# Optimization experiments

Measured on AMD Instinct MI355X. Metric: run time of the kernel, lower is better.

The kernel has to match this reference:

```python
import jax, jax.numpy as jnp
import numpy as np

B, T, F, H = 128, 256, 64, 512

def glorot(key, shape):
    fan_in, fan_out = shape[0], shape[1]
    lim = jnp.sqrt(6.0 / (fan_in + fan_out))
    return jax.random.uniform(key, shape, jnp.float32, -lim, lim)

def setup_inputs() -> dict:
    key = jax.random.key(0)
    ks = jax.random.split(key, 8)
    x = jax.random.normal(ks[0], (B, T, F), jnp.float32)
    W1 = glorot(ks[1], (F, H)); b1 = jnp.zeros((H,), jnp.float32)
    Wx1 = glorot(ks[2], (H, 4 * H)); Wh1 = glorot(ks[3], (H, 4 * H))
    blstm1 = jnp.concatenate([jnp.zeros((H,)), jnp.ones((H,)), jnp.zeros((2 * H,))]).astype(jnp.float32)  # keras unit_forget_bias
    Wx2 = glorot(ks[4], (H, 4 * H)); Wh2 = glorot(ks[5], (H, 4 * H))
    blstm2 = jnp.concatenate([jnp.zeros((H,)), jnp.ones((H,)), jnp.zeros((2 * H,))]).astype(jnp.float32)
    gamma = jnp.ones((H,), jnp.float32); beta = jnp.zeros((H,), jnp.float32)
    W2 = glorot(ks[6], (H, H // 2)); b2 = jnp.zeros((H // 2,), jnp.float32)
    W3 = glorot(ks[7], (H // 2, 1)); b3 = jnp.zeros((1,), jnp.float32)
    return dict(x=x, W1=W1, b1=b1, Wx1=Wx1, Wh1=Wh1, blstm1=blstm1,
                Wx2=Wx2, Wh2=Wh2, blstm2=blstm2, gamma=gamma, beta=beta,
                W2=W2, b2=b2, W3=W3, b3=b3)

def lstm(x, Wx, Wh, b):
    # x: [B, T, Din] -> sequence of hidden states [B, T, H] and last h [B, H]
    h_dim = Wh.shape[0]
    xg = jnp.einsum('btd,dg->btg', x, Wx) + b  # precompute input contributions [B,T,4H]
    def step(carry, xt):
        h, c = carry
        g = xt + h @ Wh
        i, f, cb, o = jnp.split(g, 4, axis=-1)
        i = jax.nn.sigmoid(i); f = jax.nn.sigmoid(f); o = jax.nn.sigmoid(o)
        c = f * c + i * jnp.tanh(cb)
        h = o * jnp.tanh(c)
        return (h, c), h
    init = (jnp.zeros((x.shape[0], h_dim), x.dtype), jnp.zeros((x.shape[0], h_dim), x.dtype))
    (h_last, _), hs = jax.lax.scan(step, init, jnp.swapaxes(xg, 0, 1))
    return jnp.swapaxes(hs, 0, 1), h_last

def reference(x, W1, b1, Wx1, Wh1, blstm1, Wx2, Wh2, blstm2, gamma, beta, W2, b2, W3, b3):
    h = x @ W1 + b1                                  # dense1 [B,T,H]
    # spectral_norm lambda: L2-normalize last axis, scale by sqrt(H)
    norm = jnp.linalg.norm(h, axis=-1, keepdims=True)
    h = h / jnp.maximum(norm, 1e-12) * jnp.sqrt(jnp.float32(h.shape[-1]))
    seq, _ = lstm(h, Wx1, Wh1, blstm1)               # lstm1 return_sequences
    _, h2 = lstm(seq, Wx2, Wh2, blstm2)              # lstm2 last output [B,H]
    mu = jnp.mean(h2, axis=-1, keepdims=True)
    var = jnp.mean((h2 - mu) ** 2, axis=-1, keepdims=True)
    h2 = (h2 - mu) * jax.lax.rsqrt(var + 1e-3) * gamma + beta  # keras LayerNorm eps=1e-3
    h3 = jax.nn.relu(h2 @ W2 + b2)
    return h3 @ W3 + b3                               # [B,1]
```

## Files before the change

kernel.cpp:

```cpp
#include <hip/hip_runtime.h>
#include <hip/hip_bf16.h>
#include <math.h>

#define B_ 128
#define T_ 256
#define F_ 64
#define H_ 512
#define G4_ 2048

#define XB0_OFF 0
#define XB1_OFF 32768
#define HB_OFF  65536
#define GLD_OFF 98304
#define SMEM_TOTAL 115712

typedef __attribute__((ext_vector_type(8))) short bf16x8;
typedef __attribute__((ext_vector_type(4))) float f32x4;

__device__ __forceinline__ void coh_store_u32(unsigned* p, unsigned v) {
  __hip_atomic_store(p, v, __ATOMIC_RELAXED, __HIP_MEMORY_SCOPE_AGENT);
}
__device__ __forceinline__ unsigned coh_load_u32(const unsigned* p) {
  return __hip_atomic_load(p, __ATOMIC_RELAXED, __HIP_MEMORY_SCOPE_AGENT);
}
__device__ __forceinline__ void rawbar() { __builtin_amdgcn_s_barrier(); }

__device__ __forceinline__ void async_ld16(const void* g, void* l) {
  __builtin_amdgcn_global_load_lds(
      (const __attribute__((address_space(1))) void*)g,
      (__attribute__((address_space(3))) void*)l, 16, 0, 0);
}
__device__ __forceinline__ void async_ld16c(const void* g, void* l) {
  __builtin_amdgcn_global_load_lds(
      (const __attribute__((address_space(1))) void*)g,
      (__attribute__((address_space(3))) void*)l, 16, 0, 17);
}

__device__ __forceinline__ float fsig(float x) {
  float e = __builtin_amdgcn_exp2f(-1.44269504089f * x);
  return __builtin_amdgcn_rcpf(1.f + e);
}
__device__ __forceinline__ float ftanh(float x) {
  float ax = __builtin_fabsf(x);
  float e = __builtin_amdgcn_exp2f(-2.88539008177f * ax);
  float r = (1.f - e) * __builtin_amdgcn_rcpf(1.f + e);
  return __builtin_copysignf(r, x);
}

__global__ __launch_bounds__(256) void transpose_cast_k(
    const float* __restrict__ s0, const float* __restrict__ s1,
    const float* __restrict__ s2, const float* __restrict__ s3,
    __hip_bfloat16* __restrict__ dst)
{
  __shared__ float lds[64][65];
  const float* src = (blockIdx.z == 0) ? s0 : (blockIdx.z == 1) ? s1 : (blockIdx.z == 2) ? s2 : s3;
  __hip_bfloat16* d = dst + (size_t)blockIdx.z * (G4_ * H_);
  int n0 = blockIdx.x * 64, k0 = blockIdx.y * 64;
  int tx = threadIdx.x & 63, ty = threadIdx.x >> 6;
#pragma unroll
  for (int r = 0; r < 16; r++) { int k = r * 4 + ty; lds[k][tx] = src[(size_t)(k0 + k) * G4_ + n0 + tx]; }
  __syncthreads();
#pragma unroll
  for (int r = 0; r < 16; r++) { int n = r * 4 + ty; d[(size_t)(n0 + n) * H_ + k0 + tx] = __float2bfloat16(lds[tx][n]); }
}

__global__ void prep_misc_k(const float* __restrict__ w1, __hip_bfloat16* __restrict__ w1b,
                            float* __restrict__ zbase, int nzero)
{
  int i = blockIdx.x * blockDim.x + threadIdx.x;
  int stride = gridDim.x * blockDim.x;
  for (int k = i; k < F_ * H_; k += stride) w1b[k] = __float2bfloat16(w1[k]);
  for (int k = i; k < nzero; k += stride) zbase[k] = 0.f;
}

__global__ __launch_bounds__(512) void dense1_k(
    const float* __restrict__ x, const __hip_bfloat16* __restrict__ w1b,
    const float* __restrict__ b1, __hip_bfloat16* __restrict__ h0)
{
  __shared__ float red[8];
  int j = threadIdx.x;
  int wave = j >> 6, lane = j & 63;
  float wcol[64];
#pragma unroll
  for (int k = 0; k < 64; k++) wcol[k] = __bfloat162float(w1b[k * H_ + j]);
  float bj = b1[j];
  for (int r = 0; r < 32; r++) {
    int row = blockIdx.x * 32 + r;
    const float* xr = x + (size_t)row * F_;
    float acc = bj;
#pragma unroll
    for (int k = 0; k < 64; k++) acc += xr[k] * wcol[k];
    float ss = acc * acc;
#pragma unroll
    for (int o = 32; o; o >>= 1) ss += __shfl_down(ss, o);
    if (lane == 0) red[wave] = ss;
    __syncthreads();
    float tot = red[0] + red[1] + red[2] + red[3] + red[4] + red[5] + red[6] + red[7];
    float sc = sqrtf(512.f) / fmaxf(sqrtf(tot), 1e-12f);
    h0[(size_t)row * H_ + j] = __float2bfloat16(acc * sc);
    __syncthreads();
  }
}

#define RUN_CHAIN(BASEPTR, W0, W1, A0, A1)                                    \
  {                                                                           \
    const char* _cb = (const char*)(BASEPTR);                                 \
    _Pragma("unroll")                                                         \
    for (int kc = 0; kc < 8; kc++) {                                          \
      bf16x8 _av = *(const bf16x8*)(_cb + ((mh * 16 + kh * 8 + kc) << 10) + (lane << 4)); \
      A0 = __builtin_amdgcn_mfma_f32_16x16x32_bf16(_av, W0[kc], A0, 0, 0, 0); \
      A1 = __builtin_amdgcn_mfma_f32_16x16x32_bf16(_av, W1[kc], A1, 0, 0, 0); \
    }                                                                         \
  }

__global__ __launch_bounds__(512, 2) void lstm_fused_k(
    const __hip_bfloat16* __restrict__ h0,
    __hip_bfloat16* __restrict__ seq,
    const __hip_bfloat16* __restrict__ wh1, const __hip_bfloat16* __restrict__ wx1,
    const float* __restrict__ bl1,
    const __hip_bfloat16* __restrict__ wh2, const __hip_bfloat16* __restrict__ wx2,
    const float* __restrict__ bl2,
    __hip_bfloat16* __restrict__ h1A, __hip_bfloat16* __restrict__ h1B,
    __hip_bfloat16* __restrict__ h2A, __hip_bfloat16* __restrict__ h2B,
    float* __restrict__ h2f,
    unsigned* flags)
{
  extern __shared__ char smem[];
  float* gld = (float*)(smem + GLD_OFF);
  const int tid = threadIdx.x;
  const int wave = tid >> 6;
  const int lane = tid & 63;
  const int lr = lane & 15;
  const int lk = lane >> 4;
  const int bid = blockIdx.x;
  const int grp = bid >> 7;
  const int lid = bid & 127;
  const int bb = lid & 3;
  const int bu = lid >> 2;
  const int m0 = bb * 32;
  const int u0 = bu * 16;

  const int kh = wave >> 2;
  const int mh = (wave >> 1) & 1;
  const int gp = wave & 1;

  const __hip_bfloat16* Wht = grp ? wh2 : wh1;
  const __hip_bfloat16* Wxt = grp ? wx2 : wx1;
  const __hip_bfloat16* xsrc = grp ? (const __hip_bfloat16*)seq : h0;
  const float* bias = grp ? bl2 : bl1;
  __hip_bfloat16* hgA = grp ? h2A : h1A;
  __hip_bfloat16* hgB = grp ? h2B : h1B;
  unsigned* dflags = flags + bb * 64;
  unsigned* ownf = dflags + (grp << 5);
  const int myflag = (grp << 5) | bu;

  bf16x8 wh_0[8], wh_1[8], wx_0[8], wx_1[8];
  {
    const size_t c0 = (size_t)((gp * 2 + 0) * 512 + u0 + lr) * H_ + kh * 256 + lk * 8;
    const size_t c1 = (size_t)((gp * 2 + 1) * 512 + u0 + lr) * H_ + kh * 256 + lk * 8;
#pragma unroll
    for (int kc = 0; kc < 8; kc++) {
      wh_0[kc] = *(const bf16x8*)(Wht + c0 + kc * 32);
      wh_1[kc] = *(const bf16x8*)(Wht + c1 + kc * 32);
      wx_0[kc] = *(const bf16x8*)(Wxt + c0 + kc * 32);
      wx_1[kc] = *(const bf16x8*)(Wxt + c1 + kc * 32);
    }
#pragma unroll
    for (int kc = 0; kc < 8; kc++) {
      asm volatile("" : "+v"(wh_0[kc]), "+v"(wh_1[kc]), "+v"(wx_0[kc]), "+v"(wx_1[kc]));
    }
  }

  const int m_e = tid >> 3, up_e = tid & 7;
  float br0[2], br1[2], br2[2], br3[2];
  float2 creg = {0.f, 0.f};
  if (tid < 256) {
#pragma unroll
    for (int c = 0; c < 2; c++) {
      br0[c] = bias[0 * 512 + u0 + 2 * up_e + c];
      br1[c] = bias[1 * 512 + u0 + 2 * up_e + c];
      br2[c] = bias[2 * 512 + u0 + 2 * up_e + c];
      br3[c] = bias[3 * 512 + u0 + 2 * up_e + c];
    }
  }

  char* xb0 = smem + XB0_OFF;
  char* xb1 = smem + XB1_OFF;

  auto issue_x = [&](int t, char* xb) {
#pragma unroll
    for (int j = 0; j < 4; j++) {
      const int c = wave * 4 + j;
      const __hip_bfloat16* g = xsrc +
          ((size_t)(m0 + (c >> 4) * 16 + lr) * T_ + t) * H_ + (c & 15) * 32 + lk * 8;
      if (grp) async_ld16c(g, xb + c * 1024);
      else     async_ld16(g, xb + c * 1024);
    }
  };
  auto issue_h = [&](int u) {
#pragma unroll
    for (int j = 0; j < 4; j++) {
      const int c = wave * 4 + j;
      const int row = m0 + (c >> 4) * 16 + lr;
      const __hip_bfloat16* g;
      if (grp) {
        const __hip_bfloat16* hsrc = ((u - 1) & 1) ? hgB : hgA;
        g = hsrc + (size_t)row * H_ + (c & 15) * 32 + lk * 8;
      } else {
        g = seq + ((size_t)row * T_ + (u - 1)) * H_ + (c & 15) * 32 + lk * 8;
      }
      async_ld16c(g, smem + HB_OFF + c * 1024);
    }
  };
  auto spin32 = [&](const unsigned* base, unsigned tgt) {
    if (lane < 32) {
      const unsigned* p = base + lane;
      while (coh_load_u32(p) < tgt) __builtin_amdgcn_s_sleep(1);
    }
  };
  auto spinA = [&](int u) {
    if (lane < 32) {
      const unsigned* p = ownf + lane;
      const unsigned tgt = (unsigned)u;
      while (coh_load_u32(p) < tgt) __builtin_amdgcn_s_sleep(1);
    } else if (grp == 1 && u <= T_ - 3) {
      const unsigned* p = dflags + (lane - 32);
      const unsigned tgt = (unsigned)(u + 3);
      while (coh_load_u32(p) < tgt) __builtin_amdgcn_s_sleep(1);
    }
  };
  auto publish = [&](unsigned v) {
    if (tid == 0) coh_store_u32(&dflags[myflag], v);
  };
  auto write_gld = [&](f32x4 s0, f32x4 s1) {
    float* d0 = gld + ((kh * 4 + gp * 2 + 0) * 32 + mh * 16 + lk * 4) * 17 + lr;
    float* d1 = gld + ((kh * 4 + gp * 2 + 1) * 32 + mh * 16 + lk * 4) * 17 + lr;
#pragma unroll
    for (int r = 0; r < 4; r++) { d0[r * 17] = s0[r]; d1[r * 17] = s1[r]; }
  };
  auto elem = [&](int u, __hip_bfloat16* hout) {
    if (tid < 256) {
      float gv0[2], gv1[2], gv2[2], gv3[2];
#pragma unroll
      for (int c = 0; c < 2; c++) {
        const int o = m_e * 17 + 2 * up_e + c;
        gv0[c] = gld[(0 * 32) * 17 + o] + gld[(4 * 32) * 17 + o] + br0[c];
        gv1[c] = gld[(1 * 32) * 17 + o] + gld[(5 * 32) * 17 + o] + br1[c];
        gv2[c] = gld[(2 * 32) * 17 + o] + gld[(6 * 32) * 17 + o] + br2[c];
        gv3[c] = gld[(3 * 32) * 17 + o] + gld[(7 * 32) * 17 + o] + br3[c];
      }
      float i0 = fsig(gv0[0]), i1 = fsig(gv0[1]);
      float f0 = fsig(gv1[0]), f1 = fsig(gv1[1]);
      float cb0 = ftanh(gv2[0]), cb1 = ftanh(gv2[1]);
      float o0 = fsig(gv3[0]), o1 = fsig(gv3[1]);
      float cn0 = f0 * creg.x + i0 * cb0;
      float cn1 = f1 * creg.y + i1 * cb1;
      creg.x = cn0; creg.y = cn1;
      float hv0 = o0 * ftanh(cn0), hv1 = o1 * ftanh(cn1);
      union { __hip_bfloat16 h[2]; unsigned u32; } pk;
      pk.h[0] = __float2bfloat16(hv0);
      pk.h[1] = __float2bfloat16(hv1);
      const int row = m0 + m_e, col = u0 + 2 * up_e;
      if (grp == 0) {
        coh_store_u32((unsigned*)seq + (((size_t)row * T_ + u) * H_ + col) / 2, pk.u32);
      } else {
        coh_store_u32((unsigned*)hout + ((size_t)row * H_ + col) / 2, pk.u32);
        if (u == T_ - 1) {
          float2 hv = {hv0, hv1};
          *(float2*)(h2f + (size_t)row * H_ + col) = hv;
        }
      }
    }
  };

  f32x4 axc0 = {0.f,0.f,0.f,0.f}, axc1 = {0.f,0.f,0.f,0.f};
  f32x4 axn0, axn1, ah0, ah1;

  if (grp) spin32(dflags, 3u);
  issue_x(0, xb0);
  issue_x(1, xb1);
  asm volatile("s_waitcnt vmcnt(0)" ::: "memory");
  rawbar();
  __builtin_amdgcn_sched_barrier(0);
  RUN_CHAIN(xb0, wx_0, wx_1, axc0, axc1);
  write_gld(axc0, axc1);
  asm volatile("s_waitcnt lgkmcnt(0)" ::: "memory");
  rawbar();
  __builtin_amdgcn_sched_barrier(0);
  elem(0, hgA);
  issue_x(2, xb0);
  asm volatile("s_waitcnt vmcnt(4)" ::: "memory");
  publish(1u);
  asm volatile("s_waitcnt vmcnt(0)" ::: "memory");
  rawbar();
  __builtin_amdgcn_sched_barrier(0);
  axc0 = (f32x4){0.f,0.f,0.f,0.f}; axc1 = (f32x4){0.f,0.f,0.f,0.f};
  RUN_CHAIN(xb1, wx_0, wx_1, axc0, axc1);

  for (int u = 1; u < T_; u++) {
    __hip_bfloat16* hout = (u & 1) ? hgB : hgA;
    const bool pf = (u <= T_ - 3);

    spinA(u);
    issue_h(u);
    if (u < T_ - 1) {
      axn0 = (f32x4){0.f,0.f,0.f,0.f}; axn1 = (f32x4){0.f,0.f,0.f,0.f};
      char* xb = ((u + 1) & 1) ? xb1 : xb0;
      RUN_CHAIN(xb, wx_0, wx_1, axn0, axn1);
    }
    asm volatile("s_waitcnt vmcnt(0)" ::: "memory");
    rawbar();
    __builtin_amdgcn_sched_barrier(0);
    ah0 = (f32x4){0.f,0.f,0.f,0.f}; ah1 = (f32x4){0.f,0.f,0.f,0.f};
    RUN_CHAIN(smem + HB_OFF, wh_0, wh_1, ah0, ah1);
    write_gld(axc0 + ah0, axc1 + ah1);
    asm volatile("s_waitcnt lgkmcnt(0)" ::: "memory");
    rawbar();
    __builtin_amdgcn_sched_barrier(0);
    elem(u, hout);
    if (pf) {
      issue_x(u + 2, (u & 1) ? xb1 : xb0);
      asm volatile("s_waitcnt vmcnt(4)" ::: "memory");
      publish((unsigned)(u + 1));
      asm volatile("s_waitcnt vmcnt(0)" ::: "memory");
    } else {
      asm volatile("s_waitcnt vmcnt(0)" ::: "memory");
      publish((unsigned)(u + 1));
    }
    rawbar();
    axc0 = axn0; axc1 = axn1;
  }
}

__global__ __launch_bounds__(256) void final_k(
    const float* __restrict__ h2, const float* __restrict__ gamma, const float* __restrict__ beta,
    const float* __restrict__ W2, const float* __restrict__ b2,
    const float* __restrict__ W3, const float* __restrict__ b3, float* __restrict__ out)
{
  __shared__ float y[512];
  __shared__ float redS[4], redQ[4], redP[4];
  int b = blockIdx.x, tid = threadIdx.x;
  int wave = tid >> 6, lane = tid & 63;
  float v0 = h2[b * H_ + tid], v1 = h2[b * H_ + 256 + tid];
  float s = v0 + v1, q = v0 * v0 + v1 * v1;
#pragma unroll
  for (int o = 32; o; o >>= 1) { s += __shfl_down(s, o); q += __shfl_down(q, o); }
  if (lane == 0) { redS[wave] = s; redQ[wave] = q; }
  __syncthreads();
  float tot = redS[0] + redS[1] + redS[2] + redS[3];
  float totq = redQ[0] + redQ[1] + redQ[2] + redQ[3];
  float mu = tot * (1.f / 512.f);
  float var = totq * (1.f / 512.f) - mu * mu;
  float rs = rsqrtf(var + 1e-3f);
  y[tid]       = (v0 - mu) * rs * gamma[tid] + beta[tid];
  y[tid + 256] = (v1 - mu) * rs * gamma[tid + 256] + beta[tid + 256];
  __syncthreads();
  float acc = b2[tid];
  for (int k = 0; k < 512; k++) acc += y[k] * W2[k * 256 + tid];
  float pv = fmaxf(acc, 0.f) * W3[tid];
#pragma unroll
  for (int o = 32; o; o >>= 1) pv += __shfl_down(pv, o);
  if (lane == 0) redP[wave] = pv;
  __syncthreads();
  if (tid == 0) out[b] = redP[0] + redP[1] + redP[2] + redP[3] + b3[0];
}

extern "C" void kernel_launch(void* const* d_in, const int* in_sizes, int n_in,
                              void* d_out, int out_size, void* d_ws, size_t ws_size,
                              hipStream_t stream)
{
  (void)in_sizes; (void)n_in; (void)out_size; (void)ws_size;
  const float* x    = (const float*)d_in[0];
  const float* W1   = (const float*)d_in[1];
  const float* b1   = (const float*)d_in[2];
  const float* Wx1  = (const float*)d_in[3];
  const float* Wh1  = (const float*)d_in[4];
  const float* bl1  = (const float*)d_in[5];
  const float* Wx2  = (const float*)d_in[6];
  const float* Wh2  = (const float*)d_in[7];
  const float* bl2  = (const float*)d_in[8];
  const float* gam  = (const float*)d_in[9];
  const float* bet  = (const float*)d_in[10];
  const float* W2   = (const float*)d_in[11];
  const float* b2   = (const float*)d_in[12];
  const float* W3   = (const float*)d_in[13];
  const float* b3   = (const float*)d_in[14];

  char* p = (char*)d_ws;
  const size_t MB = 1024 * 1024;
  __hip_bfloat16* wx1t = (__hip_bfloat16*)(p + 0 * MB);
  __hip_bfloat16* wh1t = (__hip_bfloat16*)(p + 2 * MB);
  __hip_bfloat16* wx2t = (__hip_bfloat16*)(p + 4 * MB);
  __hip_bfloat16* wh2t = (__hip_bfloat16*)(p + 6 * MB);
  __hip_bfloat16* w1b  = (__hip_bfloat16*)(p + 8 * MB);
  __hip_bfloat16* h0   = (__hip_bfloat16*)(p + 9 * MB);
  __hip_bfloat16* seq  = (__hip_bfloat16*)(p + 41 * MB);
  char* st = p + 73 * MB;
  __hip_bfloat16* h1A = (__hip_bfloat16*)st;
  __hip_bfloat16* h1B = h1A + B_ * H_;
  __hip_bfloat16* h2A = h1B + B_ * H_;
  __hip_bfloat16* h2B = h2A + B_ * H_;
  float* h2f = (float*)(st + 512 * 1024);
  unsigned* flags = (unsigned*)(st + 512 * 1024 + 256 * 1024);
  int nzero = (int)((512 * 1024 + 256 * 1024 + 4096) / 4);

  transpose_cast_k<<<dim3(32, 8, 4), 256, 0, stream>>>(Wx1, Wh1, Wx2, Wh2, wx1t);
  prep_misc_k<<<256, 256, 0, stream>>>(W1, w1b, (float*)st, nzero);
  dense1_k<<<1024, 512, 0, stream>>>(x, w1b, b1, h0);

  void* args[] = { (void*)&h0, (void*)&seq,
                   (void*)&wh1t, (void*)&wx1t, (void*)&bl1,
                   (void*)&wh2t, (void*)&wx2t, (void*)&bl2,
                   (void*)&h1A, (void*)&h1B, (void*)&h2A, (void*)&h2B,
                   (void*)&h2f, (void*)&flags };
  hipLaunchCooperativeKernel((void*)lstm_fused_k, dim3(256), dim3(512), args,
                             SMEM_TOTAL, stream);

  final_k<<<128, 256, 0, stream>>>(h2f, gam, bet, W2, b2, W3, b3, (float*)d_out);
}
```

Baseline: 1.181 ms.

## Interleave gate columns per wave to do LSTM cell math in registers via swizzle

Reassigns each wave's output columns so that the four gates of a hidden unit sit in adjacent lanes. Each wave now covers the full K=512 reduction, which removes the split-K LDS staging buffer and the extra barrier before the element-wise cell update. Gate values are exchanged with ds_swizzle and each lane stores one bf16 h value. The next-step x prefetch is also issued earlier so it overlaps the h matmul. The cost is a longer serial MFMA chain per wave, narrower 16-bit stores, and redundant activation work across lanes.

```diff
diff --git a/kernel.cpp b/kernel.cpp
--- a/kernel.cpp
+++ b/kernel.cpp
@@ -11,13 +11,15 @@
 #define XB0_OFF 0
 #define XB1_OFF 32768
 #define HB_OFF  65536
-#define GLD_OFF 98304
-#define SMEM_TOTAL 115712
+#define SMEM_TOTAL 98304
 
 typedef __attribute__((ext_vector_type(8))) short bf16x8;
 typedef __attribute__((ext_vector_type(4))) float f32x4;
 
 __device__ __forceinline__ void coh_store_u32(unsigned* p, unsigned v) {
+  __hip_atomic_store(p, v, __ATOMIC_RELAXED, __HIP_MEMORY_SCOPE_AGENT);
+}
+__device__ __forceinline__ void coh_store_u16(unsigned short* p, unsigned short v) {
   __hip_atomic_store(p, v, __ATOMIC_RELAXED, __HIP_MEMORY_SCOPE_AGENT);
 }
 __device__ __forceinline__ unsigned coh_load_u32(const unsigned* p) {
@@ -45,6 +47,10 @@
   float e = __builtin_amdgcn_exp2f(-2.88539008177f * ax);
   float r = (1.f - e) * __builtin_amdgcn_rcpf(1.f + e);
   return __builtin_copysignf(r, x);
+}
+template<int PAT>
+__device__ __forceinline__ float swz(float v) {
+  return __uint_as_float(__builtin_amdgcn_ds_swizzle(__float_as_uint(v), PAT));
 }
 
 __global__ __launch_bounds__(256) void transpose_cast_k(
@@ -102,14 +108,14 @@
   }
 }
 
-#define RUN_CHAIN(BASEPTR, W0, W1, A0, A1)                                    \
+#define RUN_CHAINF(BASEPTR, W, A0, A1)                                        \
   {                                                                           \
     const char* _cb = (const char*)(BASEPTR);                                 \
     _Pragma("unroll")                                                         \
-    for (int kc = 0; kc < 8; kc++) {                                          \
-      bf16x8 _av = *(const bf16x8*)(_cb + ((mh * 16 + kh * 8 + kc) << 10) + (lane << 4)); \
-      A0 = __builtin_amdgcn_mfma_f32_16x16x32_bf16(_av, W0[kc], A0, 0, 0, 0); \
-      A1 = __builtin_amdgcn_mfma_f32_16x16x32_bf16(_av, W1[kc], A1, 0, 0, 0); \
+    for (int kc = 0; kc < 16; kc++) {                                         \
+      bf16x8 _av = *(const bf16x8*)(_cb + ((mh * 16 + kc) << 10) + (lane << 4)); \
+      if (kc & 1) A1 = __builtin_amdgcn_mfma_f32_16x16x32_bf16(_av, W[kc], A1, 0, 0, 0); \
+      else        A0 = __builtin_amdgcn_mfma_f32_16x16x32_bf16(_av, W[kc], A0, 0, 0, 0); \
     }                                                                         \
   }
 
@@ -126,7 +132,6 @@
     unsigned* flags)
 {
   extern __shared__ char smem[];
-  float* gld = (float*)(smem + GLD_OFF);
   const int tid = threadIdx.x;
   const int wave = tid >> 6;
   const int lane = tid & 63;
@@ -140,9 +145,11 @@
   const int m0 = bb * 32;
   const int u0 = bu * 16;
 
-  const int kh = wave >> 2;
-  const int mh = (wave >> 1) & 1;
-  const int gp = wave & 1;
+  const int mh = wave >> 2;
+  const int q  = wave & 3;
+  const int p  = lr & 3;
+  const int ucol = u0 + q * 4 + (lr >> 2);
+  const int pcol = p * 512 + ucol;
 
   const __hip_bfloat16* Wht = grp ? wh2 : wh1;
   const __hip_bfloat16* Wxt = grp ? wx2 : wx1;
@@ -154,35 +161,22 @@
   unsigned* ownf = dflags + (grp << 5);
   const int myflag = (grp << 5) | bu;
 
-  bf16x8 wh_0[8], wh_1[8], wx_0[8], wx_1[8];
+  bf16x8 wh_[16], wx_[16];
   {
-    const size_t c0 = (size_t)((gp * 2 + 0) * 512 + u0 + lr) * H_ + kh * 256 + lk * 8;
-    const size_t c1 = (size_t)((gp * 2 + 1) * 512 + u0 + lr) * H_ + kh * 256 + lk * 8;
-#pragma unroll
-    for (int kc = 0; kc < 8; kc++) {
-      wh_0[kc] = *(const bf16x8*)(Wht + c0 + kc * 32);
-      wh_1[kc] = *(const bf16x8*)(Wht + c1 + kc * 32);
-      wx_0[kc] = *(const bf16x8*)(Wxt + c0 + kc * 32);
-      wx_1[kc] = *(const bf16x8*)(Wxt + c1 + kc * 32);
-    }
-#pragma unroll
-    for (int kc = 0; kc < 8; kc++) {
-      asm volatile("" : "+v"(wh_0[kc]), "+v"(wh_1[kc]), "+v"(wx_0[kc]), "+v"(wx_1[kc]));
+    const __hip_bfloat16* hw = Wht + (size_t)pcol * H_ + lk * 8;
+    const __hip_bfloat16* xw = Wxt + (size_t)pcol * H_ + lk * 8;
+#pragma unroll
+    for (int kc = 0; kc < 16; kc++) {
+      wh_[kc] = *(const bf16x8*)(hw + kc * 32);
+      wx_[kc] = *(const bf16x8*)(xw + kc * 32);
+    }
+#pragma unroll
+    for (int kc = 0; kc < 16; kc++) {
+      asm volatile("" : "+v"(wh_[kc]), "+v"(wx_[kc]));
     }
   }
-
-  const int m_e = tid >> 3, up_e = tid & 7;
-  float br0[2], br1[2], br2[2], br3[2];
-  float2 creg = {0.f, 0.f};
-  if (tid < 256) {
-#pragma unroll
-    for (int c = 0; c < 2; c++) {
-      br0[c] = bias[0 * 512 + u0 + 2 * up_e + c];
-      br1[c] = bias[1 * 512 + u0 + 2 * up_e + c];
-      br2[c] = bias[2 * 512 + u0 + 2 * up_e + c];
-      br3[c] = bias[3 * 512 + u0 + 2 * up_e + c];
-    }
-  }
+  const float bias0 = bias[pcol];
+  f32x4 cst = {0.f, 0.f, 0.f, 0.f};
 
   char* xb0 = smem + XB0_OFF;
   char* xb1 = smem + XB1_OFF;
@@ -214,67 +208,58 @@
   };
   auto spin32 = [&](const unsigned* base, unsigned tgt) {
     if (lane < 32) {
-      const unsigned* p = base + lane;
-      while (coh_load_u32(p) < tgt) __builtin_amdgcn_s_sleep(1);
+      const unsigned* pp = base + lane;
+      while (coh_load_u32(pp) < tgt) __builtin_amdgcn_s_sleep(1);
     }
   };
   auto spinA = [&](int u) {
     if (lane < 32) {
-      const unsigned* p = ownf + lane;
+      const unsigned* pp = ownf + lane;
       const unsigned tgt = (unsigned)u;
-      while (coh_load_u32(p) < tgt) __builtin_amdgcn_s_sleep(1);
+      while (coh_load_u32(pp) < tgt) __builtin_amdgcn_s_sleep(1);
     } else if (grp == 1 && u <= T_ - 3) {
-      const unsigned* p = dflags + (lane - 32);
+      const unsigned* pp = dflags + (lane - 32);
       const unsigned tgt = (unsigned)(u + 3);
-      while (coh_load_u32(p) < tgt) __builtin_amdgcn_s_sleep(1);
+      while (coh_load_u32(pp) < tgt) __builtin_amdgcn_s_sleep(1);
     }
   };
   auto publish = [&](unsigned v) {
     if (tid == 0) coh_store_u32(&dflags[myflag], v);
   };
-  auto write_gld = [&](f32x4 s0, f32x4 s1) {
-    float* d0 = gld + ((kh * 4 + gp * 2 + 0) * 32 + mh * 16 + lk * 4) * 17 + lr;
-    float* d1 = gld + ((kh * 4 + gp * 2 + 1) * 32 + mh * 16 + lk * 4) * 17 + lr;
-#pragma unroll
-    for (int r = 0; r < 4; r++) { d0[r * 17] = s0[r]; d1[r * 17] = s1[r]; }
-  };
-  auto elem = [&](int u, __hip_bfloat16* hout) {
-    if (tid < 256) {
-      float gv0[2], gv1[2], gv2[2], gv3[2];
-#pragma unroll
-      for (int c = 0; c < 2; c++) {
-        const int o = m_e * 17 + 2 * up_e + c;
-        gv0[c] = gld[(0 * 32) * 17 + o] + gld[(4 * 32) * 17 + o] + br0[c];
-        gv1[c] = gld[(1 * 32) * 17 + o] + gld[(5 * 32) * 17 + o] + br1[c];
-        gv2[c] = gld[(2 * 32) * 17 + o] + gld[(6 * 32) * 17 + o] + br2[c];
-        gv3[c] = gld[(3 * 32) * 17 + o] + gld[(7 * 32) * 17 + o] + br3[c];
-      }
-      float i0 = fsig(gv0[0]), i1 = fsig(gv0[1]);
-      float f0 = fsig(gv1[0]), f1 = fsig(gv1[1]);
-      float cb0 = ftanh(gv2[0]), cb1 = ftanh(gv2[1]);
-      float o0 = fsig(gv3[0]), o1 = fsig(gv3[1]);
-      float cn0 = f0 * creg.x + i0 * cb0;
-      float cn1 = f1 * creg.y + i1 * cb1;
-      creg.x = cn0; creg.y = cn1;
-      float hv0 = o0 * ftanh(cn0), hv1 = o1 * ftanh(cn1);
-      union { __hip_bfloat16 h[2]; unsigned u32; } pk;
-      pk.h[0] = __float2bfloat16(hv0);
-      pk.h[1] = __float2bfloat16(hv1);
-      const int row = m0 + m_e, col = u0 + 2 * up_e;
-      if (grp == 0) {
-        coh_store_u32((unsigned*)seq + (((size_t)row * T_ + u) * H_ + col) / 2, pk.u32);
-      } else {
-        coh_store_u32((unsigned*)hout + ((size_t)row * H_ + col) / 2, pk.u32);
-        if (u == T_ - 1) {
-          float2 hv = {hv0, hv1};
-          *(float2*)(h2f + (size_t)row * H_ + col) = hv;
-        }
-      }
-    }
-  };
 
   f32x4 axc0 = {0.f,0.f,0.f,0.f}, axc1 = {0.f,0.f,0.f,0.f};
   f32x4 axn0, axn1, ah0, ah1;
+
+  auto elem = [&](int u, __hip_bfloat16* hout, bool with_h) {
+    float hv0 = 0.f, hv1 = 0.f, hv2 = 0.f, hv3 = 0.f;
+#pragma unroll
+    for (int r = 0; r < 4; r++) {
+      float gv = axc0[r] + axc1[r] + bias0;
+      if (with_h) gv += ah0[r] + ah1[r];
+      float act = (p == 2) ? ftanh(gv) : fsig(gv);
+      float v1 = swz<0x041F>(act);
+      float v2 = swz<0x081F>(act);
+      float v3 = swz<0x0C1F>(act);
+      float iv  = (p == 0) ? act : (p == 1) ? v1  : (p == 2) ? v2  : v3;
+      float fv  = (p == 0) ? v1  : (p == 1) ? act : (p == 2) ? v3  : v2;
+      float cbv = (p == 0) ? v2  : (p == 1) ? v3  : (p == 2) ? act : v1;
+      float ov  = (p == 0) ? v3  : (p == 1) ? v2  : (p == 2) ? v1  : act;
+      float cn = fv * cst[r] + iv * cbv;
+      cst[r] = cn;
+      float hv = ov * ftanh(cn);
+      if (r == 0) hv0 = hv; else if (r == 1) hv1 = hv;
+      else if (r == 2) hv2 = hv; else hv3 = hv;
+    }
+    float hsel = (p == 0) ? hv0 : (p == 1) ? hv1 : (p == 2) ? hv2 : hv3;
+    const int row = m0 + mh * 16 + lk * 4 + p;
+    unsigned short hb = __bfloat16_as_ushort(__float2bfloat16(hsel));
+    if (grp == 0) {
+      coh_store_u16((unsigned short*)seq + ((size_t)row * T_ + u) * H_ + ucol, hb);
+    } else {
+      coh_store_u16((unsigned short*)hout + (size_t)row * H_ + ucol, hb);
+      if (u == T_ - 1) h2f[(size_t)row * H_ + ucol] = hsel;
+    }
+  };
 
   if (grp) spin32(dflags, 3u);
   issue_x(0, xb0);
@@ -282,20 +267,15 @@
   asm volatile("s_waitcnt vmcnt(0)" ::: "memory");
   rawbar();
   __builtin_amdgcn_sched_barrier(0);
-  RUN_CHAIN(xb0, wx_0, wx_1, axc0, axc1);
-  write_gld(axc0, axc1);
-  asm volatile("s_waitcnt lgkmcnt(0)" ::: "memory");
-  rawbar();
-  __builtin_amdgcn_sched_barrier(0);
-  elem(0, hgA);
+  RUN_CHAINF(xb0, wx_, axc0, axc1);
   issue_x(2, xb0);
-  asm volatile("s_waitcnt vmcnt(4)" ::: "memory");
+  elem(0, hgA, false);
+  asm volatile("s_waitcnt vmcnt(0)" ::: "memory");
   publish(1u);
-  asm volatile("s_waitcnt vmcnt(0)" ::: "memory");
   rawbar();
   __builtin_amdgcn_sched_barrier(0);
   axc0 = (f32x4){0.f,0.f,0.f,0.f}; axc1 = (f32x4){0.f,0.f,0.f,0.f};
-  RUN_CHAIN(xb1, wx_0, wx_1, axc0, axc1);
+  RUN_CHAINF(xb1, wx_, axc0, axc1);
 
   for (int u = 1; u < T_; u++) {
     __hip_bfloat16* hout = (u & 1) ? hgB : hgA;
@@ -303,30 +283,21 @@
 
     spinA(u);
     issue_h(u);
+    if (pf) issue_x(u + 2, (u & 1) ? xb1 : xb0);
     if (u < T_ - 1) {
       axn0 = (f32x4){0.f,0.f,0.f,0.f}; axn1 = (f32x4){0.f,0.f,0.f,0.f};
       char* xb = ((u + 1) & 1) ? xb1 : xb0;
-      RUN_CHAIN(xb, wx_0, wx_1, axn0, axn1);
-    }
-    asm volatile("s_waitcnt vmcnt(0)" ::: "memory");
+      RUN_CHAINF(xb, wx_, axn0, axn1);
+    }
+    if (pf) asm volatile("s_waitcnt vmcnt(4)" ::: "memory");
+    else    asm volatile("s_waitcnt vmcnt(0)" ::: "memory");
     rawbar();
     __builtin_amdgcn_sched_barrier(0);
     ah0 = (f32x4){0.f,0.f,0.f,0.f}; ah1 = (f32x4){0.f,0.f,0.f,0.f};
-    RUN_CHAIN(smem + HB_OFF, wh_0, wh_1, ah0, ah1);
-    write_gld(axc0 + ah0, axc1 + ah1);
-    asm volatile("s_waitcnt lgkmcnt(0)" ::: "memory");
-    rawbar();
-    __builtin_amdgcn_sched_barrier(0);
-    elem(u, hout);
-    if (pf) {
-      issue_x(u + 2, (u & 1) ? xb1 : xb0);
-      asm volatile("s_waitcnt vmcnt(4)" ::: "memory");
-      publish((unsigned)(u + 1));
-      asm volatile("s_waitcnt vmcnt(0)" ::: "memory");
-    } else {
-      asm volatile("s_waitcnt vmcnt(0)" ::: "memory");
-      publish((unsigned)(u + 1));
-    }
+    RUN_CHAINF(smem + HB_OFF, wh_, ah0, ah1);
+    elem(u, hout, true);
+    asm volatile("s_waitcnt vmcnt(0)" ::: "memory");
+    publish((unsigned)(u + 1));
     rawbar();
     axc0 = axn0; axc1 = axn1;
   }
```

After: 1.455 ms. 1.23x slower.
